# Optimization experiments

Hardware: AMD Instinct MI355X
Metric: run time of the kernel (lower is better)

Reference implementation:

```python
import jax, jax.numpy as jnp
import numpy as np
import math
from jax import lax

# cfg['MODEL'] constants
MU = 0.1          # FISTA step size
LMBD = 0.1        # LAMBDA[0], sparsity weight
N_DICT = 1        # EXPANSION_FACTOR
N_STEPS = 6       # NUM_LAYERS (FISTA iterations)
K = 3             # kernel_size
PAD = 1           # padding
STRIDE = 1        # stride (POOLING=False, stride passed to conv)
DN = ('NCHW', 'OIHW', 'NCHW')


def _conv(x, w):
    # F.conv2d(x, w, stride=1, padding=PAD)
    return lax.conv_general_dilated(x, w, (STRIDE, STRIDE), [(PAD, PAD), (PAD, PAD)], dimension_numbers=DN)


def _conv_t(y, w):
    # F.conv_transpose2d(y, w, stride=1, padding=PAD) == conv2d with flipped, in/out-swapped kernel, pad K-1-PAD
    wt = jnp.transpose(jnp.flip(w, (-1, -2)), (1, 0, 2, 3))  # [Cin, Cout, K, K]
    p = K - 1 - PAD
    return lax.conv_general_dilated(y, wt, (1, 1), [(p, p), (p, p)], dimension_numbers=DN)


def _shrink(z, thr):
    # non_negative=True soft-threshold: relu(z - thr)
    return jax.nn.relu(z - thr)


def setup_inputs() -> dict:
    key = jax.random.key(0)
    k1, k2 = jax.random.split(key)
    x = jax.random.normal(k1, (16, 64, 56, 56), dtype=jnp.float32)
    # dictionary weight [out_channels, in_channels*n_dict, K, K], kaiming-ish scale
    W = jax.random.normal(k2, (128, 64 * N_DICT, K, K), dtype=jnp.float32) * 0.05
    return {"x": x, "W": W}


def reference(x, W):
    # w_norm: each output filter normalized to unit Frobenius norm
    Wn = W / jnp.sqrt(jnp.sum(W * W, axis=(1, 2, 3), keepdims=True) + 1e-12)
    thr = MU * LMBD
    xr = jnp.tile(x, (1, N_DICT, 1, 1)) if N_DICT > 1 else x

    # FISTA iteration 0: c = shrink(mu * D^T x)
    c = _shrink(MU * _conv(xr, Wn), thr)
    y = c
    c_prev = c
    t = 1.0
    for _ in range(N_STEPS - 1):
        r = xr - _conv_t(y, Wn)                       # residual x - D c
        c_new = _shrink(y + MU * _conv(r, Wn), thr)   # gradient step + shrink
        t_next = (1.0 + math.sqrt(1.0 + 4.0 * t * t)) / 2.0
        y = c_new + ((t - 1.0) / t_next) * (c_new - c_prev)  # momentum
        c_prev = c_new
        t = t_next
    # POOLING=False -> DictConv2d returns the sparse code directly
    return c_prev
```

## Files before the change

kernel.cpp:

```cpp
#include <hip/hip_runtime.h>
#include <hip/hip_bf16.h>
#include <math.h>

typedef __attribute__((ext_vector_type(8))) short short8;
typedef __attribute__((ext_vector_type(4))) float f32x4;

#define MU_  0.1f
#define THR_ 0.01f
#define ZB_  204

static __device__ inline short f2bf(float f) {
    __hip_bfloat16 h = __float2bfloat16(f);
    return *reinterpret_cast<short*>(&h);
}
static __device__ inline float bf2f(unsigned short u) {
    unsigned int x = ((unsigned int)u) << 16;
    return __builtin_bit_cast(float, x);
}

__global__ __launch_bounds__(256) void prep_kernel(
    const float* __restrict__ x, const float* __restrict__ W,
    short* __restrict__ Rp, short* __restrict__ Yp,
    short* __restrict__ Xp, short* __restrict__ Wf2, short* __restrict__ Wt2) {
    __shared__ float lx[64 * 57];
    const int bid = blockIdx.x, tid = threadIdx.x;
    if (bid < ZB_) {
        int gid = bid * 256 + tid;
        const short8 z = {0, 0, 0, 0, 0, 0, 0, 0};
        if (gid < 17408) {
            int ridx = gid / 544, off = gid - ridx * 544;
            int n = ridx >> 1, row = (ridx & 1) * 57;
            ((short8*)(Rp + ((size_t)(n * 58 + row) * 68) * 64))[off] = z;
        } else {
            int g2 = gid - 17408;
            int ridx = g2 / 1088, off = g2 - ridx * 1088;
            int n = ridx >> 1, row = (ridx & 1) * 57;
            ((short8*)(Yp + ((size_t)(n * 58 + row) * 68) * 128))[off] = z;
        }
    } else if (bid < ZB_ + 32) {
        int co = (bid - ZB_) * 4 + (tid >> 6);
        int ci = tid & 63;
        const float* wp = W + (co * 64 + ci) * 9;
        float v[9]; float s = 0.f;
#pragma unroll
        for (int t = 0; t < 9; ++t) { v[t] = wp[t]; s += v[t] * v[t]; }
#pragma unroll
        for (int off = 32; off; off >>= 1) s += __shfl_xor(s, off, 64);
        float inv = 1.0f / sqrtf(s + 1e-12f);
#pragma unroll
        for (int t = 0; t < 9; ++t) {
            Wf2[((t * 8 + (ci >> 3)) * 128 + co) * 8 + (ci & 7)] = f2bf(v[t] * inv);
            Wt2[((t * 16 + (co >> 3)) * 64 + ci) * 8 + (co & 7)] = f2bf(v[8 - t] * inv);
        }
    } else {
        int pb = bid - ZB_ - 32;
        int row = pb % 58, n = pb / 58;
        short* dst = Xp + ((size_t)(n * 58 + row) * 68) * 64;
        if (row >= 1 && row <= 56) {
            int h = row - 1;
            for (int j = tid; j < 64 * 56; j += 256) {
                int ci = j / 56, w = j - ci * 56;
                lx[ci * 57 + w] = x[((size_t)(n * 64 + ci)) * 3136 + h * 56 + w];
            }
            __syncthreads();
            for (int j = tid; j < 68 * 64; j += 256) {
                int s = j >> 6, ci = j & 63;
                float val = (s >= 2 && s < 58) ? lx[ci * 57 + (s - 2)] : 0.f;
                dst[(s << 6) + (ci ^ ((s & 7) << 3))] = f2bf(val);
            }
        } else {
            for (int j = tid; j < 68 * 64; j += 256) dst[j] = 0;
        }
    }
}

static __device__ __forceinline__ void zero_lds_pads4(short* smem, int tid) {
    const short8 z = {0, 0, 0, 0, 0, 0, 0, 0};
    for (int i = tid; i < 384; i += 256) {
        int sr = i >> 3, w = i & 7;
        int row = sr / 12, sl = sr - row * 12;
        int s = (sl < 2) ? sl : sl + 56;
        *(short8*)(smem + (row * 68 + s) * 72 + w * 8) = z;
    }
}

__global__ __launch_bounds__(256, 2) void conv_fwd(
    const short* __restrict__ inp,
    const short* __restrict__ Wf2,
    short* __restrict__ Yp,
    short* __restrict__ Cp,
    float* __restrict__ outp, int mode, float beta) {
    __shared__ __align__(16) short smem[19584];
    const int bid = blockIdx.x, tid = threadIdx.x;
    const int sid0 = (bid & 7) * 112 + (bid >> 3) * 2;
    const int n = sid0 / 56, r0 = sid0 - n * 56 + 1;
    zero_lds_pads4(smem, tid);
    {
        const short8* src = (const short8*)(inp + ((size_t)(n * 58 + (r0 - 1)) * 68) * 64);
        for (int j = tid; j < 1792; j += 256) {
            int sr = j >> 3, w = j & 7;
            int row = sr / 56, s = sr - row * 56 + 2;
            *(short8*)(smem + (row * 68 + s) * 72 + w * 8) = src[(row * 68 + s) * 8 + w];
        }
    }
    const int lane = tid & 63, ct = tid >> 6, quad = lane >> 4, l15 = lane & 15;
    const int cog = ct & 1, pxg = ct >> 1;
    size_t prow[2];
    prow[0] = ((size_t)(n * 58 + r0) * 68) * 128;
    prow[1] = prow[0] + 68 * 128;

    short8 yold8[2][2], cold8[2][2];
    int pvv[2], pg[2]; bool pok[2];
#pragma unroll
    for (int k = 0; k < 2; ++k) {
        int item = tid + k * 256;
        pok[k] = item < 448;
        pvv[k] = item >> 3; pg[k] = item & 7;
        if (mode != 0 && pok[k]) {
            int s = pvv[k] + 2;
            int xo = 8 * (pg[k] ^ (s & 7));
#pragma unroll
            for (int rw = 0; rw < 2; ++rw) {
                size_t off = prow[rw] + (size_t)s * 128 + xo;
                yold8[rw][k] = *(const short8*)(Yp + off);
                if (mode == 1) cold8[rw][k] = *(const short8*)(Cp + off);
            }
        }
    }
    __syncthreads();

    f32x4 acc[2][2][4];
#pragma unroll
    for (int rw = 0; rw < 2; ++rw)
#pragma unroll
        for (int pt = 0; pt < 2; ++pt)
#pragma unroll
            for (int cot = 0; cot < 4; ++cot) acc[rw][pt][cot] = (f32x4){0.f, 0.f, 0.f, 0.f};

#pragma unroll
    for (int f = 0; f < 18; ++f) {
        const int t = f >> 1, half = f & 1;
        const int dh = t / 3, dw = t % 3;
        const int u = l15 + dw + 1;
        const int phys = (half * 4 + quad) ^ (u & 7);
        short8 areg[4];
#pragma unroll
        for (int cot = 0; cot < 4; ++cot) {
            const int co = cog * 64 + cot * 16 + l15;
            areg[cot] = *(const short8*)(Wf2 +
                ((size_t)((t * 8 + half * 4 + quad) * 128 + co)) * 8);
        }
#pragma unroll
        for (int rw = 0; rw < 2; ++rw) {
#pragma unroll
            for (int pt = 0; pt < 2; ++pt) {
                const int pti = pxg * 2 + pt;
                const short8 bv = *(const short8*)(smem +
                    ((dh + rw) * 68 + pti * 16 + u) * 72 + phys * 8);
#pragma unroll
                for (int cot = 0; cot < 4; ++cot)
                    acc[rw][pt][cot] = __builtin_amdgcn_mfma_f32_16x16x32_bf16(areg[cot], bv, acc[rw][pt][cot], 0, 0, 0);
            }
        }
    }

    __syncthreads();
    short* tbase = smem;
    const int h0 = r0 - 1;
#pragma unroll
    for (int hh = 0; hh < 2; ++hh) {
        if (mode != 0) {
#pragma unroll
            for (int rw = 0; rw < 2; ++rw) {
                short* tb_y = tbase + rw * 9216;
                short* tb_c = tb_y + 4608;
#pragma unroll
                for (int k = 0; k < 2; ++k) if (pok[k]) {
                    int o = pvv[k] * 72 + 8 * (pg[k] ^ (pvv[k] & 3));
                    *(short8*)(tb_y + o) = yold8[rw][k];
                    if (mode == 1) *(short8*)(tb_c + o) = cold8[rw][k];
                }
            }
        }
        __syncthreads();
        if (hh == 0 && mode != 0) {
#pragma unroll
            for (int k = 0; k < 2; ++k) if (pok[k]) {
                int s = pvv[k] + 2;
                int xo = 8 * ((pg[k] + 8) ^ (s & 7));
#pragma unroll
                for (int rw = 0; rw < 2; ++rw) {
                    size_t off = prow[rw] + (size_t)s * 128 + xo;
                    yold8[rw][k] = *(const short8*)(Yp + off);
                    if (mode == 1) cold8[rw][k] = *(const short8*)(Cp + off);
                }
            }
        }
        if (cog == hh) {
#pragma unroll
            for (int rw = 0; rw < 2; ++rw) {
                short* tb_y = tbase + rw * 9216;
                short* tb_c = tb_y + 4608;
#pragma unroll
                for (int pt = 0; pt < 2; ++pt) {
                    const int px = pxg * 32 + pt * 16 + l15;
#pragma unroll
                    for (int cot = 0; cot < 4; ++cot) {
#pragma unroll
                        for (int reg = 0; reg < 4; ++reg) {
                            const int lch = cot * 16 + quad * 4 + reg;
                            const int slot = px * 72 + (lch ^ ((px & 3) << 3));
                            const float a = acc[rw][pt][cot][reg];
                            if (mode == 0) {
                                float c = fmaxf(MU_ * a - THR_, 0.f);
                                short cb16 = f2bf(c);
                                tb_y[slot] = cb16;
                                tb_c[slot] = cb16;
                            } else if (mode == 1) {
                                float yold = bf2f((unsigned short)tb_y[slot]);
                                float cold = bf2f((unsigned short)tb_c[slot]);
                                float c = fmaxf(yold + MU_ * a - THR_, 0.f);
                                tb_y[slot] = f2bf(c + beta * (c - cold));
                                tb_c[slot] = f2bf(c);
                            } else {
                                if (px < 56) {
                                    float yold = bf2f((unsigned short)tb_y[slot]);
                                    float c = fmaxf(yold + MU_ * a - THR_, 0.f);
                                    outp[((size_t)(n * 128 + hh * 64 + lch)) * 3136 + (h0 + rw) * 56 + px] = c;
                                }
                            }
                        }
                    }
                }
            }
        }
        if (mode != 2) {
            __syncthreads();
            for (int item = tid; item < 448; item += 256) {
                int vv = item >> 3, g = item & 7;
                int so = vv * 72 + 8 * (g ^ (vv & 3));
                int s = vv + 2;
                int xo = 8 * ((g + 8 * hh) ^ (s & 7));
#pragma unroll
                for (int rw = 0; rw < 2; ++rw) {
                    short* tb_y = tbase + rw * 9216;
                    short8 yv = *(const short8*)(tb_y + so);
                    short8 cv = *(const short8*)(tb_y + 4608 + so);
                    size_t off = prow[rw] + (size_t)s * 128 + xo;
                    *(short8*)(Yp + off) = yv;
                    *(short8*)(Cp + off) = cv;
                }
            }
        }
        if (hh == 0) __syncthreads();
    }
}

__global__ __launch_bounds__(256, 2) void conv_t(
    const short* __restrict__ Ypb,
    const short* __restrict__ Wt2,
    const short* __restrict__ Xp,
    short* __restrict__ Rp) {
    __shared__ __align__(16) short smem[19584];
    const int bid = blockIdx.x, tid = threadIdx.x;
    const int sid0 = (bid & 7) * 112 + (bid >> 3) * 2;
    const int n = sid0 / 56, r0 = sid0 - n * 56 + 1;
    const int lane = tid & 63, ct = tid >> 6, quad = lane >> 4, l15 = lane & 15;
    const short8* src = (const short8*)(Ypb + ((size_t)(n * 58 + (r0 - 1)) * 68) * 128);
    size_t prowX[2];
    prowX[0] = ((size_t)(n * 58 + r0) * 68) * 64;
    prowX[1] = prowX[0] + 68 * 64;

    short8 xold8[2][2];
    int pvv[2], pg[2]; bool pok[2];
#pragma unroll
    for (int k = 0; k < 2; ++k) {
        int item = tid + k * 256;
        pok[k] = item < 448;
        pvv[k] = item >> 3; pg[k] = item & 7;
        if (pok[k]) {
            int s = pvv[k] + 2;
            int xo = 8 * (pg[k] ^ (s & 7));
#pragma unroll
            for (int rw = 0; rw < 2; ++rw)
                xold8[rw][k] = *(const short8*)(Xp + prowX[rw] + (size_t)s * 64 + xo);
        }
    }

    zero_lds_pads4(smem, tid);
    for (int j = tid; j < 1792; j += 256) {
        int sr = j >> 3, w = j & 7;
        int row = sr / 56, s = sr - row * 56 + 2;
        *(short8*)(smem + (row * 68 + s) * 72 + w * 8) = src[(row * 68 + s) * 16 + w];
    }

    f32x4 acc[2][4];
#pragma unroll
    for (int rw = 0; rw < 2; ++rw)
#pragma unroll
        for (int cit = 0; cit < 4; ++cit) acc[rw][cit] = (f32x4){0.f, 0.f, 0.f, 0.f};

    __syncthreads();

    short8 pf[7];
#pragma unroll
    for (int k = 0; k < 7; ++k) {
        int j = tid + k * 256;
        if (j < 1792) {
            int sr = j >> 3, w = j & 7;
            int row = sr / 56, s = sr - row * 56 + 2;
            pf[k] = src[(row * 68 + s) * 16 + 8 + w];
        }
    }

#pragma unroll
    for (int p = 0; p < 2; ++p) {
        if (p) {
            __syncthreads();
#pragma unroll
            for (int k = 0; k < 7; ++k) {
                int j = tid + k * 256;
                if (j < 1792) {
                    int sr = j >> 3, w = j & 7;
                    int row = sr / 56, s = sr - row * 56 + 2;
                    *(short8*)(smem + (row * 68 + s) * 72 + w * 8) = pf[k];
                }
            }
            __syncthreads();
        }
#pragma unroll
        for (int f = 0; f < 18; ++f) {
            const int t = f >> 1, sh = f & 1;
            const int dh = t / 3, dw = t % 3;
            const int u = l15 + dw + 1;
            const int phys = (sh * 4 + quad) ^ (u & 7);
            short8 areg[4];
#pragma unroll
            for (int cit = 0; cit < 4; ++cit) {
                const int ci = cit * 16 + l15;
                areg[cit] = *(const short8*)(Wt2 +
                    ((size_t)((t * 16 + (p * 2 + sh) * 4 + quad) * 64 + ci)) * 8);
            }
#pragma unroll
            for (int rw = 0; rw < 2; ++rw) {
                const short8 bv = *(const short8*)(smem +
                    ((dh + rw) * 68 + ct * 16 + u) * 72 + phys * 8);
#pragma unroll
                for (int cit = 0; cit < 4; ++cit)
                    acc[rw][cit] = __builtin_amdgcn_mfma_f32_16x16x32_bf16(areg[cit], bv, acc[rw][cit], 0, 0, 0);
            }
        }
    }

    __syncthreads();
    short* tbase = smem;
#pragma unroll
    for (int rw = 0; rw < 2; ++rw) {
#pragma unroll
        for (int k = 0; k < 2; ++k) if (pok[k]) {
            *(short8*)(tbase + rw * 4608 + pvv[k] * 72 + 8 * (pg[k] ^ (pvv[k] & 3))) = xold8[rw][k];
        }
    }
    __syncthreads();
    {
        const int px = ct * 16 + l15;
#pragma unroll
        for (int rw = 0; rw < 2; ++rw) {
            short* tb = tbase + rw * 4608;
#pragma unroll
            for (int cit = 0; cit < 4; ++cit) {
#pragma unroll
                for (int reg = 0; reg < 4; ++reg) {
                    const int cir = cit * 16 + quad * 4 + reg;
                    const int slot = px * 72 + (cir ^ ((px & 3) << 3));
                    float xo = bf2f((unsigned short)tb[slot]);
                    tb[slot] = f2bf(xo - acc[rw][cit][reg]);
                }
            }
        }
    }
    __syncthreads();
    for (int item = tid; item < 448; item += 256) {
        int vv = item >> 3, g = item & 7;
        int so = vv * 72 + 8 * (g ^ (vv & 3));
        int s = vv + 2;
        int xo = 8 * (g ^ (s & 7));
#pragma unroll
        for (int rw = 0; rw < 2; ++rw) {
            short8 val = *(const short8*)(tbase + rw * 4608 + so);
            *(short8*)(Rp + prowX[rw] + (size_t)s * 64 + xo) = val;
        }
    }
}

extern "C" void kernel_launch(void* const* d_in, const int* in_sizes, int n_in,
                              void* d_out, int out_size, void* d_ws, size_t ws_size,
                              hipStream_t stream) {
    const float* x = (const float*)d_in[0];
    const float* W = (const float*)d_in[1];
    float* out = (float*)d_out;

    const size_t XPN = (size_t)16 * 58 * 68 * 64;
    const size_t YPN = 2 * XPN;
    short* Xp = (short*)d_ws;
    short* Rp = Xp + XPN;
    short* Yp = Rp + XPN;
    short* Cp = Yp + YPN;
    short* Wf2 = Cp + YPN;
    short* Wt2 = Wf2 + 73728;

    const int prep_blocks = ZB_ + 32 + 58 * 16;
    hipLaunchKernelGGL(prep_kernel, dim3(prep_blocks), dim3(256), 0, stream,
                       x, W, Rp, Yp, Xp, Wf2, Wt2);

    dim3 b(256, 1, 1);
    hipLaunchKernelGGL(conv_fwd, dim3(448), b, 0, stream, Xp, Wf2, Yp, Cp,
                       (float*)nullptr, 0, 0.f);
    double t = 1.0;
    for (int it = 1; it <= 5; ++it) {
        hipLaunchKernelGGL(conv_t, dim3(448), b, 0, stream, Yp, Wt2, Xp, Rp);
        double tn = (1.0 + sqrt(1.0 + 4.0 * t * t)) / 2.0;
        float beta = (float)((t - 1.0) / tn);
        hipLaunchKernelGGL(conv_fwd, dim3(448), b, 0, stream, Rp, Wf2, Yp, Cp,
                           (it == 5) ? out : (float*)nullptr, (it == 5) ? 2 : 1,
                           beta);
        t = tn;
    }
}
```

Measured before the change: 345.4 us.

## Fuse transpose-conv residual and forward conv into one kernel with halo recompute

Each FISTA iteration's conv_t and conv_fwd launches are merged into a single conv_fused kernel. It computes the residual for 6 rows (4 output rows plus halo) straight into LDS and then runs the forward conv from there, so the residual buffer never goes to global memory. Y is now double-buffered (YA/YB) so the in-place update cannot race with neighbouring blocks reading halo rows. The cost is halo recompute (6 residual rows per 4 outputs), larger LDS use with launch_bounds occupancy 1, and only 224 blocks, which may underfill the GPU.

```diff
diff --git a/kernel.cpp b/kernel.cpp
--- a/kernel.cpp
+++ b/kernel.cpp
@@ -7,7 +7,7 @@
 
 #define MU_  0.1f
 #define THR_ 0.01f
-#define ZB_  204
+#define ZB_  272
 
 static __device__ inline short f2bf(float f) {
     __hip_bfloat16 h = __float2bfloat16(f);
@@ -20,23 +20,18 @@
 
 __global__ __launch_bounds__(256) void prep_kernel(
     const float* __restrict__ x, const float* __restrict__ W,
-    short* __restrict__ Rp, short* __restrict__ Yp,
+    short* __restrict__ YA, short* __restrict__ YB,
     short* __restrict__ Xp, short* __restrict__ Wf2, short* __restrict__ Wt2) {
     __shared__ float lx[64 * 57];
     const int bid = blockIdx.x, tid = threadIdx.x;
     if (bid < ZB_) {
         int gid = bid * 256 + tid;
         const short8 z = {0, 0, 0, 0, 0, 0, 0, 0};
-        if (gid < 17408) {
-            int ridx = gid / 544, off = gid - ridx * 544;
-            int n = ridx >> 1, row = (ridx & 1) * 57;
-            ((short8*)(Rp + ((size_t)(n * 58 + row) * 68) * 64))[off] = z;
-        } else {
-            int g2 = gid - 17408;
-            int ridx = g2 / 1088, off = g2 - ridx * 1088;
-            int n = ridx >> 1, row = (ridx & 1) * 57;
-            ((short8*)(Yp + ((size_t)(n * 58 + row) * 68) * 128))[off] = z;
-        }
+        short* Yb = (gid < 34816) ? YA : YB;
+        int g2 = (gid < 34816) ? gid : gid - 34816;
+        int ridx = g2 / 1088, off = g2 - ridx * 1088;
+        int n = ridx >> 1, row = (ridx & 1) * 57;
+        ((short8*)(Yb + ((size_t)(n * 58 + row) * 68) * 128))[off] = z;
     } else if (bid < ZB_ + 32) {
         int co = (bid - ZB_) * 4 + (tid >> 6);
         int ci = tid & 63;
@@ -88,8 +83,7 @@
     const short* __restrict__ inp,
     const short* __restrict__ Wf2,
     short* __restrict__ Yp,
-    short* __restrict__ Cp,
-    float* __restrict__ outp, int mode, float beta) {
+    short* __restrict__ Cp) {
     __shared__ __align__(16) short smem[19584];
     const int bid = blockIdx.x, tid = threadIdx.x;
     const int sid0 = (bid & 7) * 112 + (bid >> 3) * 2;
@@ -108,25 +102,6 @@
     size_t prow[2];
     prow[0] = ((size_t)(n * 58 + r0) * 68) * 128;
     prow[1] = prow[0] + 68 * 128;
-
-    short8 yold8[2][2], cold8[2][2];
-    int pvv[2], pg[2]; bool pok[2];
-#pragma unroll
-    for (int k = 0; k < 2; ++k) {
-        int item = tid + k * 256;
-        pok[k] = item < 448;
-        pvv[k] = item >> 3; pg[k] = item & 7;
-        if (mode != 0 && pok[k]) {
-            int s = pvv[k] + 2;
-            int xo = 8 * (pg[k] ^ (s & 7));
-#pragma unroll
-            for (int rw = 0; rw < 2; ++rw) {
-                size_t off = prow[rw] + (size_t)s * 128 + xo;
-                yold8[rw][k] = *(const short8*)(Yp + off);
-                if (mode == 1) cold8[rw][k] = *(const short8*)(Cp + off);
-            }
-        }
-    }
     __syncthreads();
 
     f32x4 acc[2][2][4];
@@ -166,36 +141,8 @@
 
     __syncthreads();
     short* tbase = smem;
-    const int h0 = r0 - 1;
 #pragma unroll
     for (int hh = 0; hh < 2; ++hh) {
-        if (mode != 0) {
-#pragma unroll
-            for (int rw = 0; rw < 2; ++rw) {
-                short* tb_y = tbase + rw * 9216;
-                short* tb_c = tb_y + 4608;
-#pragma unroll
-                for (int k = 0; k < 2; ++k) if (pok[k]) {
-                    int o = pvv[k] * 72 + 8 * (pg[k] ^ (pvv[k] & 3));
-                    *(short8*)(tb_y + o) = yold8[rw][k];
-                    if (mode == 1) *(short8*)(tb_c + o) = cold8[rw][k];
-                }
-            }
-        }
-        __syncthreads();
-        if (hh == 0 && mode != 0) {
-#pragma unroll
-            for (int k = 0; k < 2; ++k) if (pok[k]) {
-                int s = pvv[k] + 2;
-                int xo = 8 * ((pg[k] + 8) ^ (s & 7));
-#pragma unroll
-                for (int rw = 0; rw < 2; ++rw) {
-                    size_t off = prow[rw] + (size_t)s * 128 + xo;
-                    yold8[rw][k] = *(const short8*)(Yp + off);
-                    if (mode == 1) cold8[rw][k] = *(const short8*)(Cp + off);
-                }
-            }
-        }
         if (cog == hh) {
 #pragma unroll
             for (int rw = 0; rw < 2; ++rw) {
@@ -210,123 +157,110 @@
                         for (int reg = 0; reg < 4; ++reg) {
                             const int lch = cot * 16 + quad * 4 + reg;
                             const int slot = px * 72 + (lch ^ ((px & 3) << 3));
-                            const float a = acc[rw][pt][cot][reg];
-                            if (mode == 0) {
-                                float c = fmaxf(MU_ * a - THR_, 0.f);
-                                short cb16 = f2bf(c);
-                                tb_y[slot] = cb16;
-                                tb_c[slot] = cb16;
-                            } else if (mode == 1) {
-                                float yold = bf2f((unsigned short)tb_y[slot]);
-                                float cold = bf2f((unsigned short)tb_c[slot]);
-                                float c = fmaxf(yold + MU_ * a - THR_, 0.f);
-                                tb_y[slot] = f2bf(c + beta * (c - cold));
-                                tb_c[slot] = f2bf(c);
-                            } else {
-                                if (px < 56) {
-                                    float yold = bf2f((unsigned short)tb_y[slot]);
-                                    float c = fmaxf(yold + MU_ * a - THR_, 0.f);
-                                    outp[((size_t)(n * 128 + hh * 64 + lch)) * 3136 + (h0 + rw) * 56 + px] = c;
-                                }
-                            }
+                            float c = fmaxf(MU_ * acc[rw][pt][cot][reg] - THR_, 0.f);
+                            short cb16 = f2bf(c);
+                            tb_y[slot] = cb16;
+                            tb_c[slot] = cb16;
                         }
                     }
                 }
             }
         }
-        if (mode != 2) {
-            __syncthreads();
-            for (int item = tid; item < 448; item += 256) {
-                int vv = item >> 3, g = item & 7;
-                int so = vv * 72 + 8 * (g ^ (vv & 3));
-                int s = vv + 2;
-                int xo = 8 * ((g + 8 * hh) ^ (s & 7));
-#pragma unroll
-                for (int rw = 0; rw < 2; ++rw) {
-                    short* tb_y = tbase + rw * 9216;
-                    short8 yv = *(const short8*)(tb_y + so);
-                    short8 cv = *(const short8*)(tb_y + 4608 + so);
-                    size_t off = prow[rw] + (size_t)s * 128 + xo;
-                    *(short8*)(Yp + off) = yv;
-                    *(short8*)(Cp + off) = cv;
-                }
+        __syncthreads();
+        for (int item = tid; item < 448; item += 256) {
+            int vv = item >> 3, g = item & 7;
+            int so = vv * 72 + 8 * (g ^ (vv & 3));
+            int s = vv + 2;
+            int xo = 8 * ((g + 8 * hh) ^ (s & 7));
+#pragma unroll
+            for (int rw = 0; rw < 2; ++rw) {
+                short* tb_y = tbase + rw * 9216;
+                short8 yv = *(const short8*)(tb_y + so);
+                short8 cv = *(const short8*)(tb_y + 4608 + so);
+                size_t off = prow[rw] + (size_t)s * 128 + xo;
+                *(short8*)(Yp + off) = yv;
+                *(short8*)(Cp + off) = cv;
             }
         }
         if (hh == 0) __syncthreads();
     }
 }
 
-__global__ __launch_bounds__(256, 2) void conv_t(
-    const short* __restrict__ Ypb,
+__global__ __launch_bounds__(256, 1) void conv_fused(
+    const short* __restrict__ Ycur,
     const short* __restrict__ Wt2,
+    const short* __restrict__ Wf2,
     const short* __restrict__ Xp,
-    short* __restrict__ Rp) {
-    __shared__ __align__(16) short smem[19584];
+    short* __restrict__ Ynext,
+    short* __restrict__ Cp,
+    float* __restrict__ outp, int mode, float beta) {
+    __shared__ __align__(16) short smem[68544];
+    short* win = smem;
+    short* Rt  = smem + 39168;
     const int bid = blockIdx.x, tid = threadIdx.x;
-    const int sid0 = (bid & 7) * 112 + (bid >> 3) * 2;
+    const int sid0 = (bid & 7) * 112 + (bid >> 3) * 4;
     const int n = sid0 / 56, r0 = sid0 - n * 56 + 1;
     const int lane = tid & 63, ct = tid >> 6, quad = lane >> 4, l15 = lane & 15;
-    const short8* src = (const short8*)(Ypb + ((size_t)(n * 58 + (r0 - 1)) * 68) * 128);
-    size_t prowX[2];
-    prowX[0] = ((size_t)(n * 58 + r0) * 68) * 64;
-    prowX[1] = prowX[0] + 68 * 64;
-
-    short8 xold8[2][2];
+    const short8 z8 = {0, 0, 0, 0, 0, 0, 0, 0};
+
+    for (int i = tid; i < 768; i += 256) {
+        int sr = i >> 3, w = i & 7;
+        int wr = sr / 12, sl = sr - wr * 12;
+        int s = (sl < 2) ? sl : sl + 56;
+        *(short8*)(win + (wr * 68 + s) * 72 + w * 8) = z8;
+    }
+    for (int i = tid; i < 576; i += 256) {
+        int sr = i >> 3, w = i & 7;
+        int rr = sr / 12, sl = sr - rr * 12;
+        int s = (sl < 2) ? sl : sl + 56;
+        *(short8*)(Rt + (rr * 68 + s) * 72 + w * 8) = z8;
+    }
+
     int pvv[2], pg[2]; bool pok[2];
 #pragma unroll
     for (int k = 0; k < 2; ++k) {
         int item = tid + k * 256;
         pok[k] = item < 448;
         pvv[k] = item >> 3; pg[k] = item & 7;
-        if (pok[k]) {
-            int s = pvv[k] + 2;
-            int xo = 8 * (pg[k] ^ (s & 7));
-#pragma unroll
-            for (int rw = 0; rw < 2; ++rw)
-                xold8[rw][k] = *(const short8*)(Xp + prowX[rw] + (size_t)s * 64 + xo);
-        }
-    }
-
-    zero_lds_pads4(smem, tid);
-    for (int j = tid; j < 1792; j += 256) {
-        int sr = j >> 3, w = j & 7;
-        int row = sr / 56, s = sr - row * 56 + 2;
-        *(short8*)(smem + (row * 68 + s) * 72 + w * 8) = src[(row * 68 + s) * 16 + w];
-    }
-
-    f32x4 acc[2][4];
-#pragma unroll
-    for (int rw = 0; rw < 2; ++rw)
-#pragma unroll
-        for (int cit = 0; cit < 4; ++cit) acc[rw][cit] = (f32x4){0.f, 0.f, 0.f, 0.f};
-
-    __syncthreads();
-
-    short8 pf[7];
-#pragma unroll
-    for (int k = 0; k < 7; ++k) {
-        int j = tid + k * 256;
-        if (j < 1792) {
+    }
+
+    f32x4 acc3[3][2][4];
+#pragma unroll
+    for (int p3 = 0; p3 < 3; ++p3)
+#pragma unroll
+        for (int rw = 0; rw < 2; ++rw)
+#pragma unroll
+            for (int cit = 0; cit < 4; ++cit) acc3[p3][rw][cit] = (f32x4){0.f, 0.f, 0.f, 0.f};
+
+    short8 xold[3][2][2];
+#pragma unroll
+    for (int p = 0; p < 2; ++p) {
+        if (p) __syncthreads();
+        for (int j = tid; j < 3584; j += 256) {
             int sr = j >> 3, w = j & 7;
-            int row = sr / 56, s = sr - row * 56 + 2;
-            pf[k] = src[(row * 68 + s) * 16 + 8 + w];
-        }
-    }
-
-#pragma unroll
-    for (int p = 0; p < 2; ++p) {
-        if (p) {
-            __syncthreads();
-#pragma unroll
-            for (int k = 0; k < 7; ++k) {
-                int j = tid + k * 256;
-                if (j < 1792) {
-                    int sr = j >> 3, w = j & 7;
-                    int row = sr / 56, s = sr - row * 56 + 2;
-                    *(short8*)(smem + (row * 68 + s) * 72 + w * 8) = pf[k];
-                }
-            }
-            __syncthreads();
+            int wr = sr / 56, s = sr - wr * 56 + 2;
+            int gr = r0 - 2 + wr;
+            short8 v = z8;
+            if (gr >= 0 && gr <= 57)
+                v = *(const short8*)(Ycur +
+                    ((size_t)(n * 58 + gr) * 68 + s) * 128 + p * 64 + w * 8);
+            *(short8*)(win + (wr * 68 + s) * 72 + w * 8) = v;
+        }
+        __syncthreads();
+        if (p == 1) {
+#pragma unroll
+            for (int p3 = 0; p3 < 3; ++p3)
+#pragma unroll
+                for (int rw = 0; rw < 2; ++rw) {
+                    int gr = r0 - 1 + 2 * p3 + rw;
+                    size_t xrow = ((size_t)(n * 58 + gr) * 68) * 64;
+#pragma unroll
+                    for (int k = 0; k < 2; ++k) if (pok[k]) {
+                        int s = pvv[k] + 2;
+                        xold[p3][rw][k] = *(const short8*)(Xp + xrow +
+                            (size_t)s * 64 + 8 * (pg[k] ^ (s & 7)));
+                    }
+                }
         }
 #pragma unroll
         for (int f = 0; f < 18; ++f) {
@@ -336,59 +270,202 @@
             const int phys = (sh * 4 + quad) ^ (u & 7);
             short8 areg[4];
 #pragma unroll
-            for (int cit = 0; cit < 4; ++cit) {
-                const int ci = cit * 16 + l15;
+            for (int cit = 0; cit < 4; ++cit)
                 areg[cit] = *(const short8*)(Wt2 +
-                    ((size_t)((t * 16 + (p * 2 + sh) * 4 + quad) * 64 + ci)) * 8);
-            }
-#pragma unroll
-            for (int rw = 0; rw < 2; ++rw) {
-                const short8 bv = *(const short8*)(smem +
-                    ((dh + rw) * 68 + ct * 16 + u) * 72 + phys * 8);
+                    ((size_t)((t * 16 + (p * 2 + sh) * 4 + quad) * 64 + cit * 16 + l15)) * 8);
+#pragma unroll
+            for (int p3 = 0; p3 < 3; ++p3)
+#pragma unroll
+                for (int rw = 0; rw < 2; ++rw) {
+                    const short8 bv = *(const short8*)(win +
+                        ((2 * p3 + rw + dh) * 68 + ct * 16 + u) * 72 + phys * 8);
+#pragma unroll
+                    for (int cit = 0; cit < 4; ++cit)
+                        acc3[p3][rw][cit] = __builtin_amdgcn_mfma_f32_16x16x32_bf16(areg[cit], bv, acc3[p3][rw][cit], 0, 0, 0);
+                }
+        }
+    }
+
+    __syncthreads();
+    short* tb = smem;
+#pragma unroll
+    for (int p3 = 0; p3 < 3; ++p3) {
+#pragma unroll
+        for (int rw = 0; rw < 2; ++rw)
+#pragma unroll
+            for (int k = 0; k < 2; ++k) if (pok[k])
+                *(short8*)(tb + rw * 4608 + pvv[k] * 72 + 8 * (pg[k] ^ (pvv[k] & 3))) = xold[p3][rw][k];
+        __syncthreads();
+        {
+            const int px = ct * 16 + l15;
+#pragma unroll
+            for (int rw = 0; rw < 2; ++rw) {
+                short* tbr = tb + rw * 4608;
 #pragma unroll
                 for (int cit = 0; cit < 4; ++cit)
-                    acc[rw][cit] = __builtin_amdgcn_mfma_f32_16x16x32_bf16(areg[cit], bv, acc[rw][cit], 0, 0, 0);
-            }
-        }
-    }
-
-    __syncthreads();
-    short* tbase = smem;
-#pragma unroll
-    for (int rw = 0; rw < 2; ++rw) {
+#pragma unroll
+                    for (int reg = 0; reg < 4; ++reg) {
+                        const int cir = cit * 16 + quad * 4 + reg;
+                        const int slot = px * 72 + (cir ^ ((px & 3) << 3));
+                        float xv = bf2f((unsigned short)tbr[slot]);
+                        tbr[slot] = f2bf(xv - acc3[p3][rw][cit][reg]);
+                    }
+            }
+        }
+        __syncthreads();
+        for (int item = tid; item < 448; item += 256) {
+            int vv = item >> 3, g = item & 7;
+            int so = vv * 72 + 8 * (g ^ (vv & 3));
+            int s = vv + 2;
+#pragma unroll
+            for (int rw = 0; rw < 2; ++rw) {
+                int gr = r0 - 1 + 2 * p3 + rw;
+                short8 val = (gr >= 1 && gr <= 56)
+                    ? *(const short8*)(tb + rw * 4608 + so) : z8;
+                *(short8*)(Rt + ((2 * p3 + rw) * 68 + s) * 72 + 8 * (g ^ (s & 7))) = val;
+            }
+        }
+        __syncthreads();
+    }
+
+    const int cog = ct & 1, pxg = ct >> 1;
+#pragma unroll
+    for (int fp = 0; fp < 2; ++fp) {
+        const int q0 = r0 + 2 * fp;
+        size_t prow[2];
+        prow[0] = ((size_t)(n * 58 + q0) * 68) * 128;
+        prow[1] = prow[0] + 68 * 128;
+
+        short8 yold8[2][2], cold8[2][2];
 #pragma unroll
         for (int k = 0; k < 2; ++k) if (pok[k]) {
-            *(short8*)(tbase + rw * 4608 + pvv[k] * 72 + 8 * (pg[k] ^ (pvv[k] & 3))) = xold8[rw][k];
-        }
-    }
-    __syncthreads();
-    {
-        const int px = ct * 16 + l15;
-#pragma unroll
-        for (int rw = 0; rw < 2; ++rw) {
-            short* tb = tbase + rw * 4608;
-#pragma unroll
-            for (int cit = 0; cit < 4; ++cit) {
-#pragma unroll
-                for (int reg = 0; reg < 4; ++reg) {
-                    const int cir = cit * 16 + quad * 4 + reg;
-                    const int slot = px * 72 + (cir ^ ((px & 3) << 3));
-                    float xo = bf2f((unsigned short)tb[slot]);
-                    tb[slot] = f2bf(xo - acc[rw][cit][reg]);
-                }
-            }
-        }
-    }
-    __syncthreads();
-    for (int item = tid; item < 448; item += 256) {
-        int vv = item >> 3, g = item & 7;
-        int so = vv * 72 + 8 * (g ^ (vv & 3));
-        int s = vv + 2;
-        int xo = 8 * (g ^ (s & 7));
-#pragma unroll
-        for (int rw = 0; rw < 2; ++rw) {
-            short8 val = *(const short8*)(tbase + rw * 4608 + so);
-            *(short8*)(Rp + prowX[rw] + (size_t)s * 64 + xo) = val;
+            int s = pvv[k] + 2;
+            int xo = 8 * (pg[k] ^ (s & 7));
+#pragma unroll
+            for (int rw = 0; rw < 2; ++rw) {
+                size_t off = prow[rw] + (size_t)s * 128 + xo;
+                yold8[rw][k] = *(const short8*)(Ycur + off);
+                if (mode == 1) cold8[rw][k] = *(const short8*)(Cp + off);
+            }
+        }
+
+        f32x4 acc[2][2][4];
+#pragma unroll
+        for (int rw = 0; rw < 2; ++rw)
+#pragma unroll
+            for (int pt = 0; pt < 2; ++pt)
+#pragma unroll
+                for (int cot = 0; cot < 4; ++cot) acc[rw][pt][cot] = (f32x4){0.f, 0.f, 0.f, 0.f};
+
+#pragma unroll
+        for (int f = 0; f < 18; ++f) {
+            const int t = f >> 1, half = f & 1;
+            const int dh = t / 3, dw = t % 3;
+            const int u = l15 + dw + 1;
+            const int phys = (half * 4 + quad) ^ (u & 7);
+            short8 areg[4];
+#pragma unroll
+            for (int cot = 0; cot < 4; ++cot) {
+                const int co = cog * 64 + cot * 16 + l15;
+                areg[cot] = *(const short8*)(Wf2 +
+                    ((size_t)((t * 8 + half * 4 + quad) * 128 + co)) * 8);
+            }
+#pragma unroll
+            for (int rw = 0; rw < 2; ++rw) {
+#pragma unroll
+                for (int pt = 0; pt < 2; ++pt) {
+                    const int pti = pxg * 2 + pt;
+                    const short8 bv = *(const short8*)(Rt +
+                        ((2 * fp + rw + dh) * 68 + pti * 16 + u) * 72 + phys * 8);
+#pragma unroll
+                    for (int cot = 0; cot < 4; ++cot)
+                        acc[rw][pt][cot] = __builtin_amdgcn_mfma_f32_16x16x32_bf16(areg[cot], bv, acc[rw][pt][cot], 0, 0, 0);
+                }
+            }
+        }
+
+        __syncthreads();
+        short* tbase = smem;
+        const int h0 = q0 - 1;
+#pragma unroll
+        for (int hh = 0; hh < 2; ++hh) {
+#pragma unroll
+            for (int rw = 0; rw < 2; ++rw) {
+                short* tb_y = tbase + rw * 9216;
+                short* tb_c = tb_y + 4608;
+#pragma unroll
+                for (int k = 0; k < 2; ++k) if (pok[k]) {
+                    int o = pvv[k] * 72 + 8 * (pg[k] ^ (pvv[k] & 3));
+                    *(short8*)(tb_y + o) = yold8[rw][k];
+                    if (mode == 1) *(short8*)(tb_c + o) = cold8[rw][k];
+                }
+            }
+            __syncthreads();
+            if (hh == 0) {
+#pragma unroll
+                for (int k = 0; k < 2; ++k) if (pok[k]) {
+                    int s = pvv[k] + 2;
+                    int xo = 8 * ((pg[k] + 8) ^ (s & 7));
+#pragma unroll
+                    for (int rw = 0; rw < 2; ++rw) {
+                        size_t off = prow[rw] + (size_t)s * 128 + xo;
+                        yold8[rw][k] = *(const short8*)(Ycur + off);
+                        if (mode == 1) cold8[rw][k] = *(const short8*)(Cp + off);
+                    }
+                }
+            }
+            if (cog == hh) {
+#pragma unroll
+                for (int rw = 0; rw < 2; ++rw) {
+                    short* tb_y = tbase + rw * 9216;
+                    short* tb_c = tb_y + 4608;
+#pragma unroll
+                    for (int pt = 0; pt < 2; ++pt) {
+                        const int px = pxg * 32 + pt * 16 + l15;
+#pragma unroll
+                        for (int cot = 0; cot < 4; ++cot) {
+#pragma unroll
+                            for (int reg = 0; reg < 4; ++reg) {
+                                const int lch = cot * 16 + quad * 4 + reg;
+                                const int slot = px * 72 + (lch ^ ((px & 3) << 3));
+                                const float a = acc[rw][pt][cot][reg];
+                                if (mode == 1) {
+                                    float yold = bf2f((unsigned short)tb_y[slot]);
+                                    float cold = bf2f((unsigned short)tb_c[slot]);
+                                    float c = fmaxf(yold + MU_ * a - THR_, 0.f);
+                                    tb_y[slot] = f2bf(c + beta * (c - cold));
+                                    tb_c[slot] = f2bf(c);
+                                } else {
+                                    if (px < 56) {
+                                        float yold = bf2f((unsigned short)tb_y[slot]);
+                                        float c = fmaxf(yold + MU_ * a - THR_, 0.f);
+                                        outp[((size_t)(n * 128 + hh * 64 + lch)) * 3136 + (h0 + rw) * 56 + px] = c;
+                                    }
+                                }
+                            }
+                        }
+                    }
+                }
+            }
+            if (mode == 1) {
+                __syncthreads();
+                for (int item = tid; item < 448; item += 256) {
+                    int vv = item >> 3, g = item & 7;
+                    int so = vv * 72 + 8 * (g ^ (vv & 3));
+                    int s = vv + 2;
+                    int xo = 8 * ((g + 8 * hh) ^ (s & 7));
+#pragma unroll
+                    for (int rw = 0; rw < 2; ++rw) {
+                        short* tb_y = tbase + rw * 9216;
+                        short8 yv = *(const short8*)(tb_y + so);
+                        short8 cv = *(const short8*)(tb_y + 4608 + so);
+                        size_t off = prow[rw] + (size_t)s * 128 + xo;
+                        *(short8*)(Ynext + off) = yv;
+                        *(short8*)(Cp + off) = cv;
+                    }
+                }
+            }
+            __syncthreads();
         }
     }
 }
@@ -403,27 +480,28 @@
     const size_t XPN = (size_t)16 * 58 * 68 * 64;
     const size_t YPN = 2 * XPN;
     short* Xp = (short*)d_ws;
-    short* Rp = Xp + XPN;
-    short* Yp = Rp + XPN;
-    short* Cp = Yp + YPN;
+    short* YA = Xp + XPN;
+    short* YB = YA + YPN;
+    short* Cp = YB + YPN;
     short* Wf2 = Cp + YPN;
     short* Wt2 = Wf2 + 73728;
 
     const int prep_blocks = ZB_ + 32 + 58 * 16;
     hipLaunchKernelGGL(prep_kernel, dim3(prep_blocks), dim3(256), 0, stream,
-                       x, W, Rp, Yp, Xp, Wf2, Wt2);
+                       x, W, YA, YB, Xp, Wf2, Wt2);
 
     dim3 b(256, 1, 1);
-    hipLaunchKernelGGL(conv_fwd, dim3(448), b, 0, stream, Xp, Wf2, Yp, Cp,
-                       (float*)nullptr, 0, 0.f);
+    hipLaunchKernelGGL(conv_fwd, dim3(448), b, 0, stream, Xp, Wf2, YA, Cp);
     double t = 1.0;
     for (int it = 1; it <= 5; ++it) {
-        hipLaunchKernelGGL(conv_t, dim3(448), b, 0, stream, Yp, Wt2, Xp, Rp);
         double tn = (1.0 + sqrt(1.0 + 4.0 * t * t)) / 2.0;
         float beta = (float)((t - 1.0) / tn);
-        hipLaunchKernelGGL(conv_fwd, dim3(448), b, 0, stream, Rp, Wf2, Yp, Cp,
-                           (it == 5) ? out : (float*)nullptr, (it == 5) ? 2 : 1,
-                           beta);
+        short* Ycur  = (it & 1) ? YA : YB;
+        short* Ynext = (it & 1) ? YB : YA;
+        hipLaunchKernelGGL(conv_fused, dim3(224), b, 0, stream,
+                           Ycur, Wt2, Wf2, Xp, Ynext, Cp,
+                           (it == 5) ? out : (float*)nullptr,
+                           (it == 5) ? 2 : 1, beta);
         t = tn;
     }
 }
```

Result: slower. 430.7 us (+24.7%).
